# Kernel tuning notes

Hardware: AMD Instinct MI355X
Metric: run time of the kernel (lower is better)

Reference implementation:

```python
import jax, jax.numpy as jnp
import numpy as np
from jax import lax

B, FEA, C, DIM_OUT, HEADS, H, W = 4, 3, 256, 256, 8, 32, 32
EPS = 1e-5


def setup_inputs() -> dict:
    key = jax.random.key(0)
    ks = jax.random.split(key, 10)
    return {
        "x": jax.random.normal(ks[0], (B, C, H, W), jnp.float32),
        "query": jax.random.normal(ks[1], (B, FEA * H * W, C), jnp.float32),
        "conv_q_w": jax.random.normal(ks[2], (FEA, C, 1, 3, 3), jnp.float32) * 0.1,
        "bn_q_gamma": jnp.ones((FEA, C), jnp.float32),
        "bn_q_beta": jnp.zeros((FEA, C), jnp.float32),
        "bn_q_mean": jnp.zeros((FEA, C), jnp.float32),
        "bn_q_var": jnp.ones((FEA, C), jnp.float32),
        "conv_k_w": jax.random.normal(ks[3], (C, 1, 3, 3), jnp.float32) * 0.1,
        "bn_k_gamma": jnp.ones((C,), jnp.float32),
        "bn_k_beta": jnp.zeros((C,), jnp.float32),
        "bn_k_mean": jnp.zeros((C,), jnp.float32),
        "bn_k_var": jnp.ones((C,), jnp.float32),
        "conv_v_w": jax.random.normal(ks[4], (C, 1, 3, 3), jnp.float32) * 0.1,
        "bn_v_gamma": jnp.ones((C,), jnp.float32),
        "bn_v_beta": jnp.zeros((C,), jnp.float32),
        "bn_v_mean": jnp.zeros((C,), jnp.float32),
        "bn_v_var": jnp.ones((C,), jnp.float32),
        "proj_q_w": jax.random.normal(ks[5], (DIM_OUT, C), jnp.float32) * 0.02,
        "proj_k_w": jax.random.normal(ks[6], (DIM_OUT, C), jnp.float32) * 0.02,
        "proj_v_w": jax.random.normal(ks[7], (DIM_OUT, C), jnp.float32) * 0.02,
        "proj_w": jax.random.normal(ks[8], (DIM_OUT, DIM_OUT), jnp.float32) * 0.02,
        "proj_b": jnp.zeros((DIM_OUT,), jnp.float32),
        "h": H,
        "w": W,
    }


def _dw_conv_bn(x, w, gamma, beta, mean, var):
    # x: [B, C, H, W]; w: [C, 1, 3, 3] depthwise; BN in eval mode (running stats)
    y = lax.conv_general_dilated(
        x, w, window_strides=(1, 1), padding="SAME",
        feature_group_count=x.shape[1],
        dimension_numbers=("NCHW", "OIHW", "NCHW"))
    inv = gamma * lax.rsqrt(var + EPS)
    return y * inv[None, :, None, None] + (beta - mean * inv)[None, :, None, None]


def reference(x, query, conv_q_w, bn_q_gamma, bn_q_beta, bn_q_mean, bn_q_var,
              conv_k_w, bn_k_gamma, bn_k_beta, bn_k_mean, bn_k_var,
              conv_v_w, bn_v_gamma, bn_v_beta, bn_v_mean, bn_v_var,
              proj_q_w, proj_k_w, proj_v_w, proj_w, proj_b, h, w):
    b, c = x.shape[0], x.shape[1]
    res = h * w
    # split query into fea_no maps, depthwise conv + BN each, concat tokens
    q_parts = []
    for i in range(FEA):
        qi = query[:, res * i:res * (i + 1), :].reshape(b, h, w, c).transpose(0, 3, 1, 2)
        qi = _dw_conv_bn(qi, conv_q_w[i], bn_q_gamma[i], bn_q_beta[i], bn_q_mean[i], bn_q_var[i])
        q_parts.append(qi.reshape(b, c, res).transpose(0, 2, 1))  # [B, h*w, C]
    q_tok = jnp.concatenate(q_parts, axis=1)                      # [B, FEA*h*w, C]
    k_tok = _dw_conv_bn(x, conv_k_w, bn_k_gamma, bn_k_beta, bn_k_mean, bn_k_var)
    k_tok = k_tok.reshape(b, c, res).transpose(0, 2, 1)           # [B, h*w, C]
    v_tok = _dw_conv_bn(x, conv_v_w, bn_v_gamma, bn_v_beta, bn_v_mean, bn_v_var)
    v_tok = v_tok.reshape(b, c, res).transpose(0, 2, 1)
    hd = DIM_OUT // HEADS
    q = (q_tok @ proj_q_w.T).reshape(b, -1, HEADS, hd).transpose(0, 2, 1, 3)  # [B,H,L,d]
    k = (k_tok @ proj_k_w.T).reshape(b, -1, HEADS, hd).transpose(0, 2, 1, 3)  # [B,H,T,d]
    v = (v_tok @ proj_v_w.T).reshape(b, -1, HEADS, hd).transpose(0, 2, 1, 3)
    scale = DIM_OUT ** (-0.5)  # note: original scales by dim_out, not head_dim
    attn = jax.nn.softmax(jnp.einsum("bhld,bhtd->bhlt", q, k) * scale, axis=-1)
    out = jnp.einsum("bhlt,bhtd->bhld", attn, v)
    out = out.transpose(0, 2, 1, 3).reshape(b, -1, DIM_OUT)
    return out @ proj_w.T + proj_b
```

## Files before the change

### kernel.cpp

```cpp
#include <hip/hip_runtime.h>
#include <hip/hip_bf16.h>
#include <math.h>

#define B_     4
#define C_     256
#define RES_   1024
#define FEA_   3
#define LQ_    3072
#define HEADS_ 8
#define EPS_   1e-5f

typedef __bf16 bf16x8 __attribute__((ext_vector_type(8)));
typedef float  f32x16 __attribute__((ext_vector_type(16)));
typedef unsigned int uint4e __attribute__((ext_vector_type(4)));

#if __has_builtin(__builtin_amdgcn_exp2f)
#define EXP2(x) __builtin_amdgcn_exp2f(x)
#else
#define EXP2(x) exp2f(x)
#endif

__device__ __forceinline__ unsigned short bfbits(float v) {
    return __builtin_bit_cast(unsigned short, (__bf16)v);
}
__device__ __forceinline__ unsigned int pkbf(float lo, float hi2) {
    return (unsigned int)bfbits(lo) | ((unsigned int)bfbits(hi2) << 16);
}

__global__ __launch_bounds__(256) void pre_kernel(
    const float* __restrict__ query, const float* __restrict__ x,
    const float* __restrict__ wq,
    const float* __restrict__ gq, const float* __restrict__ bq,
    const float* __restrict__ mq, const float* __restrict__ vq,
    const float* __restrict__ wk, const float* __restrict__ gk, const float* __restrict__ bk,
    const float* __restrict__ mk, const float* __restrict__ vk,
    const float* __restrict__ wv, const float* __restrict__ gv, const float* __restrict__ bv,
    const float* __restrict__ mv, const float* __restrict__ vv,
    const float* __restrict__ pw0, const float* __restrict__ pw1,
    const float* __restrict__ pw2, const float* __restrict__ pw3,
    __bf16* __restrict__ q_tok, float* __restrict__ k_tok, float* __restrict__ v_tok,
    __bf16* __restrict__ Wq, __bf16* __restrict__ Wk,
    __bf16* __restrict__ Wv, __bf16* __restrict__ Wo)
{
    __shared__ float plane[RES_];
    int blk = blockIdx.x, tid = threadIdx.x;

    if (blk < 3072) {
        int b = blk / 768, rem = blk % 768;
        int part = rem >> 8, rem2 = rem & 255;
        int y = rem2 >> 3, x0 = (rem2 & 7) * 4;
        int c = tid;
        const float* wp = wq + (size_t)(part * 256 + c) * 9;
        const float* qb = query + ((size_t)b * LQ_ + (size_t)part * 1024) * 256 + c;

        float w[9];
#pragma unroll
        for (int i = 0; i < 9; ++i) w[i] = wp[i];

        float v[3][6];
#pragma unroll
        for (int ky = 0; ky < 3; ++ky) {
            int yy = y + ky - 1;
#pragma unroll
            for (int kx = 0; kx < 6; ++kx) {
                int xx = x0 - 1 + kx;
                bool ok = ((unsigned)yy < 32u) && ((unsigned)xx < 32u);
                v[ky][kx] = ok ? qb[(size_t)(yy * 32 + xx) * 256] : 0.f;
            }
        }
        int gi = part * 256 + c;
        float inv = gq[gi] * rsqrtf(vq[gi] + EPS_);
        float sh  = bq[gi] - mq[gi] * inv;
#pragma unroll
        for (int xi = 0; xi < 4; ++xi) {
            float acc = 0.f;
#pragma unroll
            for (int ky = 0; ky < 3; ++ky)
#pragma unroll
                for (int kj = 0; kj < 3; ++kj)
                    acc = fmaf(w[ky * 3 + kj], v[ky][xi + kj], acc);
            int l = part * 1024 + y * 32 + x0 + xi;
            q_tok[((size_t)b * LQ_ + l) * 256 + c] = (__bf16)fmaf(acc, inv, sh);
        }
    } else if (blk < 5120) {
        int idx = blk - 3072;
        int c = idx & 255, b = (idx >> 8) & 3, which = idx >> 10;
        const float* xp = x + ((size_t)b * 256 + c) * RES_;
#pragma unroll
        for (int i = 0; i < 4; ++i) plane[tid + i * 256] = xp[tid + i * 256];
        __syncthreads();

        const float* wp = (which ? wv : wk) + (size_t)c * 9;
        float w[9];
#pragma unroll
        for (int i = 0; i < 9; ++i) w[i] = wp[i];
        float inv = (which ? gv : gk)[c] * rsqrtf((which ? vv : vk)[c] + EPS_);
        float sh  = (which ? bv : bk)[c] - (which ? mv : mk)[c] * inv;
        float* out = (which ? v_tok : k_tok) + ((size_t)b * 256 + c) * RES_;
#pragma unroll
        for (int i0 = 0; i0 < 4; ++i0) {
            int p = tid + i0 * 256;
            int y = p >> 5, xx = p & 31;
            float acc = 0.f;
#pragma unroll
            for (int ky = 0; ky < 3; ++ky) {
                int yy = y + ky - 1;
                if ((unsigned)yy >= 32u) continue;
#pragma unroll
                for (int kx = 0; kx < 3; ++kx) {
                    int x2 = xx + kx - 1;
                    if ((unsigned)x2 >= 32u) continue;
                    acc = fmaf(w[ky * 3 + kx], plane[yy * 32 + x2], acc);
                }
            }
            out[p] = fmaf(acc, inv, sh);
        }
    } else {
        int idx = blk - 5120;
        int m = idx >> 6;
        const float* s = m == 0 ? pw0 : m == 1 ? pw1 : m == 2 ? pw2 : pw3;
        __bf16*      d = m == 0 ? Wq  : m == 1 ? Wk  : m == 2 ? Wv  : Wo;
        int i = ((idx & 63) * 256 + tid) * 4;
        float4 v = *(const float4*)(s + i);
        ushort4 u;
        u.x = bfbits(v.x); u.y = bfbits(v.y); u.z = bfbits(v.z); u.w = bfbits(v.w);
        *(ushort4*)(d + i) = u;
    }
}

__global__ __launch_bounds__(256) void gemm_qkv_kernel(
    const __bf16* __restrict__ qt, const float* __restrict__ kt, const float* __restrict__ vt,
    const __bf16* __restrict__ Wq, const __bf16* __restrict__ Wk, const __bf16* __restrict__ Wv,
    __bf16* __restrict__ Qb, __bf16* __restrict__ Kb, __bf16* __restrict__ VT)
{
    int tid = threadIdx.x, lane = tid & 63, l31 = lane & 31, hi = lane >> 5;
    int gid = blockIdx.x * 4 + (tid >> 6);

    f32x16 acc;
#pragma unroll
    for (int r = 0; r < 16; ++r) acc[r] = 0.f;

    if (gid < 3072) {
        int b = gid / 768, rem = gid % 768;
        int j0 = (rem >> 3) * 32, i0 = (rem & 7) * 32;
        const __bf16* Bp = qt + ((size_t)b * LQ_ + j0 + l31) * 256 + 8 * hi;
        const __bf16* Ap = Wq + (size_t)(i0 + l31) * 256 + 8 * hi;
#pragma unroll
        for (int k0 = 0; k0 < 256; k0 += 16) {
            acc = __builtin_amdgcn_mfma_f32_32x32x16_bf16(
                *(const bf16x8*)(Ap + k0), *(const bf16x8*)(Bp + k0), acc, 0, 0, 0);
        }
        const float scale = 0.0625f * 1.44269504f;
        int head = i0 >> 5;
        __bf16* op = Qb + ((size_t)(b * HEADS_ + head) * LQ_ + j0 + l31) * 32 + 4 * hi;
#pragma unroll
        for (int rr = 0; rr < 4; ++rr) {
            ushort4 u;
            u.x = bfbits(acc[4 * rr + 0] * scale); u.y = bfbits(acc[4 * rr + 1] * scale);
            u.z = bfbits(acc[4 * rr + 2] * scale); u.w = bfbits(acc[4 * rr + 3] * scale);
            *(ushort4*)(op + 8 * rr) = u;
        }
    } else if (gid < 4096) {
        int g = gid - 3072;
        int b = g >> 8, rem = g & 255;
        int j0 = (rem >> 3) * 32, i0 = (rem & 7) * 32;
        const float* Bbase = kt + (size_t)b * 256 * RES_ + j0 + l31;
        const __bf16* Ap = Wk + (size_t)(i0 + l31) * 256 + 8 * hi;
#pragma unroll
        for (int k0 = 0; k0 < 256; k0 += 16) {
            bf16x8 bfr;
#pragma unroll
            for (int jj = 0; jj < 8; ++jj)
                bfr[jj] = (__bf16)Bbase[(size_t)(k0 + 8 * hi + jj) * RES_];
            acc = __builtin_amdgcn_mfma_f32_32x32x16_bf16(
                *(const bf16x8*)(Ap + k0), bfr, acc, 0, 0, 0);
        }
        int head = i0 >> 5;
        __bf16* op = Kb + ((size_t)(b * HEADS_ + head) * RES_ + j0 + l31) * 32 + 4 * hi;
#pragma unroll
        for (int rr = 0; rr < 4; ++rr) {
            ushort4 u;
            u.x = bfbits(acc[4 * rr + 0]); u.y = bfbits(acc[4 * rr + 1]);
            u.z = bfbits(acc[4 * rr + 2]); u.w = bfbits(acc[4 * rr + 3]);
            *(ushort4*)(op + 8 * rr) = u;
        }
    } else {
        int g = gid - 4096;
        int b = g >> 8, rem = g & 255;
        int i0t = (rem >> 3) * 32, j0 = (rem & 7) * 32;
        const float* Abase = vt + (size_t)b * 256 * RES_ + i0t + l31;
        const __bf16* Bp = Wv + (size_t)(j0 + l31) * 256 + 8 * hi;
#pragma unroll
        for (int k0 = 0; k0 < 256; k0 += 16) {
            bf16x8 afr;
#pragma unroll
            for (int jj = 0; jj < 8; ++jj)
                afr[jj] = (__bf16)Abase[(size_t)(k0 + 8 * hi + jj) * RES_];
            acc = __builtin_amdgcn_mfma_f32_32x32x16_bf16(
                afr, *(const bf16x8*)(Bp + k0), acc, 0, 0, 0);
        }
        int head = j0 >> 5;
        __bf16* op = VT + ((size_t)(b * HEADS_ + head) * 32 + l31) * RES_ + i0t + 4 * hi;
#pragma unroll
        for (int rr = 0; rr < 4; ++rr) {
            ushort4 u;
            u.x = bfbits(acc[4 * rr + 0]); u.y = bfbits(acc[4 * rr + 1]);
            u.z = bfbits(acc[4 * rr + 2]); u.w = bfbits(acc[4 * rr + 3]);
            *(ushort4*)(op + 8 * rr) = u;
        }
    }
}

__global__ __launch_bounds__(256) void gemm_out_kernel(
    const __bf16* __restrict__ Oc, const __bf16* __restrict__ Wo,
    const float* __restrict__ bias, float* __restrict__ out)
{
    int tid = threadIdx.x, lane = tid & 63, l31 = lane & 31, hi = lane >> 5;
    int gid = blockIdx.x * 4 + (tid >> 6);
    int b = gid / 768, rem = gid % 768;
    int j0 = (rem >> 3) * 32, i0 = (rem & 7) * 32;
    const __bf16* Bp = Oc + ((size_t)b * LQ_ + j0 + l31) * 256 + 8 * hi;
    const __bf16* Ap = Wo + (size_t)(i0 + l31) * 256 + 8 * hi;

    f32x16 acc;
#pragma unroll
    for (int r = 0; r < 16; ++r) acc[r] = 0.f;
#pragma unroll
    for (int k0 = 0; k0 < 256; k0 += 16) {
        acc = __builtin_amdgcn_mfma_f32_32x32x16_bf16(
            *(const bf16x8*)(Ap + k0), *(const bf16x8*)(Bp + k0), acc, 0, 0, 0);
    }
    float* op = out + ((size_t)b * LQ_ + j0 + l31) * 256 + i0 + 4 * hi;
#pragma unroll
    for (int rr = 0; rr < 4; ++rr) {
        float4 bv = *(const float4*)(bias + i0 + 4 * hi + 8 * rr);
        float4 r4;
        r4.x = acc[4 * rr + 0] + bv.x; r4.y = acc[4 * rr + 1] + bv.y;
        r4.z = acc[4 * rr + 2] + bv.z; r4.w = acc[4 * rr + 3] + bv.w;
        *(float4*)(op + 8 * rr) = r4;
    }
}

__global__ __launch_bounds__(256) void attn_mfma_kernel(
    const __bf16* __restrict__ Qb, const __bf16* __restrict__ Kb,
    const __bf16* __restrict__ VT, __bf16* __restrict__ Oc)
{
    __shared__ float Os[3][64][35];
    int tid  = threadIdx.x;
    int lane = tid & 63, l31 = lane & 31, hi = lane >> 5;
    int th   = tid >> 6;

    int i    = blockIdx.x;
    int xcd  = i & 7, slot = i >> 3;
    int bh   = xcd * 4 + slot / 48;
    int q0   = (slot % 48) * 64;

    const __bf16* qpA = Qb + ((size_t)bh * LQ_ + q0 + l31) * 32 + 8 * hi;
    bf16x8 qA0 = *(const bf16x8*)qpA;
    bf16x8 qA1 = *(const bf16x8*)(qpA + 16);
    bf16x8 qB0 = *(const bf16x8*)(qpA + 1024);
    bf16x8 qB1 = *(const bf16x8*)(qpA + 1040);

    const __bf16* kp = Kb + ((size_t)bh * RES_ + th * 256 + l31) * 32 + 8 * hi;
    const __bf16* vp = VT + ((size_t)bh * 32 + l31) * RES_ + th * 256 + 8 * hi;

    f32x16 oA, oB;
#pragma unroll
    for (int r = 0; r < 16; ++r) { oA[r] = 0.f; oB[r] = 0.f; }
    float lsA = 0.f, lsB = 0.f;

    auto smpack = [&](const f32x16& s, float& ls, bf16x8& pb1, bf16x8& pb2) {
        float p[16];
#pragma unroll
        for (int r = 0; r < 16; ++r) p[r] = EXP2(s[r]);
#pragma unroll
        for (int r = 0; r < 16; ++r) ls += p[r];

        unsigned int w0 = pkbf(p[0],  p[1]),  w1 = pkbf(p[2],  p[3]);
        unsigned int w2 = pkbf(p[4],  p[5]),  w3 = pkbf(p[6],  p[7]);
        unsigned int w4 = pkbf(p[8],  p[9]),  w5 = pkbf(p[10], p[11]);
        unsigned int w6 = pkbf(p[12], p[13]), w7 = pkbf(p[14], p[15]);

        asm("v_permlane32_swap_b32 %0, %1" : "+v"(w0), "+v"(w2));
        asm("v_permlane32_swap_b32 %0, %1" : "+v"(w1), "+v"(w3));
        asm("v_permlane32_swap_b32 %0, %1" : "+v"(w4), "+v"(w6));
        asm("v_permlane32_swap_b32 %0, %1" : "+v"(w5), "+v"(w7));

        uint4e b1 = { w0, w1, w2, w3 };
        uint4e b2 = { w4, w5, w6, w7 };
        pb1 = __builtin_bit_cast(bf16x8, b1);
        pb2 = __builtin_bit_cast(bf16x8, b2);
    };

#pragma unroll
    for (int st = 0; st < 8; ++st) {
        const __bf16* kc = kp + (size_t)st * 1024;
        const __bf16* vc = vp + (size_t)st * 32;
        bf16x8 K0 = *(const bf16x8*)kc;
        bf16x8 K1 = *(const bf16x8*)(kc + 16);
        bf16x8 V0 = *(const bf16x8*)vc;
        bf16x8 V1 = *(const bf16x8*)(vc + 16);

        f32x16 sA, sB;
#pragma unroll
        for (int r = 0; r < 16; ++r) { sA[r] = 0.f; sB[r] = 0.f; }
        sA = __builtin_amdgcn_mfma_f32_32x32x16_bf16(K0, qA0, sA, 0, 0, 0);
        sB = __builtin_amdgcn_mfma_f32_32x32x16_bf16(K0, qB0, sB, 0, 0, 0);
        sA = __builtin_amdgcn_mfma_f32_32x32x16_bf16(K1, qA1, sA, 0, 0, 0);
        sB = __builtin_amdgcn_mfma_f32_32x32x16_bf16(K1, qB1, sB, 0, 0, 0);

        bf16x8 pA1, pA2, pB1, pB2;
        smpack(sA, lsA, pA1, pA2);
        smpack(sB, lsB, pB1, pB2);

        oA = __builtin_amdgcn_mfma_f32_32x32x16_bf16(V0, pA1, oA, 0, 0, 0);
        oB = __builtin_amdgcn_mfma_f32_32x32x16_bf16(V0, pB1, oB, 0, 0, 0);
        oA = __builtin_amdgcn_mfma_f32_32x32x16_bf16(V1, pA2, oA, 0, 0, 0);
        oB = __builtin_amdgcn_mfma_f32_32x32x16_bf16(V1, pB2, oB, 0, 0, 0);
    }

    lsA += __shfl_xor(lsA, 32, 64);
    lsB += __shfl_xor(lsB, 32, 64);

    if (th) {
#pragma unroll
        for (int r = 0; r < 16; ++r) {
            Os[th - 1][lane][r]      = oA[r];
            Os[th - 1][lane][17 + r] = oB[r];
        }
        Os[th - 1][lane][16] = lsA;
        Os[th - 1][lane][33] = lsB;
    }
    __syncthreads();
    if (!th) {
        int b = bh >> 3, h = bh & 7;
        float lA = lsA + Os[0][lane][16] + Os[1][lane][16] + Os[2][lane][16];
        float lB = lsB + Os[0][lane][33] + Os[1][lane][33] + Os[2][lane][33];
        float invA = 1.0f / lA, invB = 1.0f / lB;
        __bf16* opA = Oc + ((size_t)b * LQ_ + q0 + l31) * 256 + h * 32 + 4 * hi;
        __bf16* opB = opA + (size_t)32 * 256;
#pragma unroll
        for (int rr = 0; rr < 4; ++rr) {
            ushort4 ua, ub;
            ua.x = bfbits((oA[4*rr+0] + Os[0][lane][4*rr+0] + Os[1][lane][4*rr+0] + Os[2][lane][4*rr+0]) * invA);
            ua.y = bfbits((oA[4*rr+1] + Os[0][lane][4*rr+1] + Os[1][lane][4*rr+1] + Os[2][lane][4*rr+1]) * invA);
            ua.z = bfbits((oA[4*rr+2] + Os[0][lane][4*rr+2] + Os[1][lane][4*rr+2] + Os[2][lane][4*rr+2]) * invA);
            ua.w = bfbits((oA[4*rr+3] + Os[0][lane][4*rr+3] + Os[1][lane][4*rr+3] + Os[2][lane][4*rr+3]) * invA);
            ub.x = bfbits((oB[4*rr+0] + Os[0][lane][17+4*rr+0] + Os[1][lane][17+4*rr+0] + Os[2][lane][17+4*rr+0]) * invB);
            ub.y = bfbits((oB[4*rr+1] + Os[0][lane][17+4*rr+1] + Os[1][lane][17+4*rr+1] + Os[2][lane][17+4*rr+1]) * invB);
            ub.z = bfbits((oB[4*rr+2] + Os[0][lane][17+4*rr+2] + Os[1][lane][17+4*rr+2] + Os[2][lane][17+4*rr+2]) * invB);
            ub.w = bfbits((oB[4*rr+3] + Os[0][lane][17+4*rr+3] + Os[1][lane][17+4*rr+3] + Os[2][lane][17+4*rr+3]) * invB);
            *(ushort4*)(opA + 8 * rr) = ua;
            *(ushort4*)(opB + 8 * rr) = ub;
        }
    }
}

extern "C" void kernel_launch(void* const* d_in, const int* in_sizes, int n_in,
                              void* d_out, int out_size, void* d_ws, size_t ws_size,
                              hipStream_t stream) {
    const float* x        = (const float*)d_in[0];
    const float* query    = (const float*)d_in[1];
    const float* conv_q_w = (const float*)d_in[2];
    const float* bn_q_g   = (const float*)d_in[3];
    const float* bn_q_b   = (const float*)d_in[4];
    const float* bn_q_m   = (const float*)d_in[5];
    const float* bn_q_v   = (const float*)d_in[6];
    const float* conv_k_w = (const float*)d_in[7];
    const float* bn_k_g   = (const float*)d_in[8];
    const float* bn_k_b   = (const float*)d_in[9];
    const float* bn_k_m   = (const float*)d_in[10];
    const float* bn_k_v   = (const float*)d_in[11];
    const float* conv_v_w = (const float*)d_in[12];
    const float* bn_v_g   = (const float*)d_in[13];
    const float* bn_v_b   = (const float*)d_in[14];
    const float* bn_v_m   = (const float*)d_in[15];
    const float* bn_v_v   = (const float*)d_in[16];
    const float* proj_q_w = (const float*)d_in[17];
    const float* proj_k_w = (const float*)d_in[18];
    const float* proj_v_w = (const float*)d_in[19];
    const float* proj_w   = (const float*)d_in[20];
    const float* proj_b   = (const float*)d_in[21];

    char* ws = (char*)d_ws;
    __bf16* q_tok = (__bf16*)(ws + 0);
    float*  k_tok = (float*) (ws + 6291456);
    float*  v_tok = (float*) (ws + 10485760);
    __bf16* Qb    = (__bf16*)(ws + 14680064);
    __bf16* Kb    = (__bf16*)(ws + 20971520);
    __bf16* VT    = (__bf16*)(ws + 23068672);
    __bf16* Wq    = (__bf16*)(ws + 25165824);
    __bf16* Wk    = (__bf16*)(ws + 25296896);
    __bf16* Wv    = (__bf16*)(ws + 25427968);
    __bf16* Wo    = (__bf16*)(ws + 25559040);
    __bf16* Oc    = q_tok;
    float*  out   = (float*)d_out;

    pre_kernel<<<dim3(5376), 256, 0, stream>>>(
        query, x, conv_q_w, bn_q_g, bn_q_b, bn_q_m, bn_q_v,
        conv_k_w, bn_k_g, bn_k_b, bn_k_m, bn_k_v,
        conv_v_w, bn_v_g, bn_v_b, bn_v_m, bn_v_v,
        proj_q_w, proj_k_w, proj_v_w, proj_w,
        q_tok, k_tok, v_tok, Wq, Wk, Wv, Wo);

    gemm_qkv_kernel<<<dim3(1280), 256, 0, stream>>>(
        q_tok, k_tok, v_tok, Wq, Wk, Wv, Qb, Kb, VT);

    attn_mfma_kernel<<<dim3(1536), 256, 0, stream>>>(Qb, Kb, VT, Oc);

    gemm_out_kernel<<<dim3(768), 256, 0, stream>>>(Oc, Wo, proj_b, out);
}
```

Measured before the change: 79.96 us.

## Tile query depthwise conv 4x4 per thread and prefetch K in attention loop

```diff
diff --git a/kernel.cpp b/kernel.cpp
--- a/kernel.cpp
+++ b/kernel.cpp
@@ -45,10 +45,10 @@
     __shared__ float plane[RES_];
     int blk = blockIdx.x, tid = threadIdx.x;
 
-    if (blk < 3072) {
-        int b = blk / 768, rem = blk % 768;
-        int part = rem >> 8, rem2 = rem & 255;
-        int y = rem2 >> 3, x0 = (rem2 & 7) * 4;
+    if (blk < 768) {
+        int b = blk / 192, rem = blk % 192;
+        int part = rem >> 6, t = rem & 63;
+        int y0 = (t >> 3) * 4, x0 = (t & 7) * 4;
         int c = tid;
         const float* wp = wq + (size_t)(part * 256 + c) * 9;
         const float* qb = query + ((size_t)b * LQ_ + (size_t)part * 1024) * 256 + c;
@@ -57,33 +57,36 @@
 #pragma unroll
         for (int i = 0; i < 9; ++i) w[i] = wp[i];
 
-        float v[3][6];
-#pragma unroll
-        for (int ky = 0; ky < 3; ++ky) {
-            int yy = y + ky - 1;
-#pragma unroll
-            for (int kx = 0; kx < 6; ++kx) {
-                int xx = x0 - 1 + kx;
+        float v[6][6];
+#pragma unroll
+        for (int iy = 0; iy < 6; ++iy) {
+            int yy = y0 - 1 + iy;
+#pragma unroll
+            for (int ix = 0; ix < 6; ++ix) {
+                int xx = x0 - 1 + ix;
                 bool ok = ((unsigned)yy < 32u) && ((unsigned)xx < 32u);
-                v[ky][kx] = ok ? qb[(size_t)(yy * 32 + xx) * 256] : 0.f;
+                v[iy][ix] = ok ? qb[(size_t)(yy * 32 + xx) * 256] : 0.f;
             }
         }
         int gi = part * 256 + c;
         float inv = gq[gi] * rsqrtf(vq[gi] + EPS_);
         float sh  = bq[gi] - mq[gi] * inv;
 #pragma unroll
-        for (int xi = 0; xi < 4; ++xi) {
-            float acc = 0.f;
-#pragma unroll
-            for (int ky = 0; ky < 3; ++ky)
-#pragma unroll
-                for (int kj = 0; kj < 3; ++kj)
-                    acc = fmaf(w[ky * 3 + kj], v[ky][xi + kj], acc);
-            int l = part * 1024 + y * 32 + x0 + xi;
-            q_tok[((size_t)b * LQ_ + l) * 256 + c] = (__bf16)fmaf(acc, inv, sh);
-        }
-    } else if (blk < 5120) {
-        int idx = blk - 3072;
+        for (int yi = 0; yi < 4; ++yi) {
+#pragma unroll
+            for (int xi = 0; xi < 4; ++xi) {
+                float acc = 0.f;
+#pragma unroll
+                for (int ky = 0; ky < 3; ++ky)
+#pragma unroll
+                    for (int kj = 0; kj < 3; ++kj)
+                        acc = fmaf(w[ky * 3 + kj], v[yi + ky][xi + kj], acc);
+                int l = part * 1024 + (y0 + yi) * 32 + x0 + xi;
+                q_tok[((size_t)b * LQ_ + l) * 256 + c] = (__bf16)fmaf(acc, inv, sh);
+            }
+        }
+    } else if (blk < 2816) {
+        int idx = blk - 768;
         int c = idx & 255, b = (idx >> 8) & 3, which = idx >> 10;
         const float* xp = x + ((size_t)b * 256 + c) * RES_;
 #pragma unroll
@@ -116,7 +119,7 @@
             out[p] = fmaf(acc, inv, sh);
         }
     } else {
-        int idx = blk - 5120;
+        int idx = blk - 2816;
         int m = idx >> 6;
         const float* s = m == 0 ? pw0 : m == 1 ? pw1 : m == 2 ? pw2 : pw3;
         __bf16*      d = m == 0 ? Wq  : m == 1 ? Wk  : m == 2 ? Wv  : Wo;
@@ -292,31 +295,44 @@
         pb2 = __builtin_bit_cast(bf16x8, b2);
     };
 
+    bf16x8 kc0 = *(const bf16x8*)kp;
+    bf16x8 kc1 = *(const bf16x8*)(kp + 16);
+
 #pragma unroll
     for (int st = 0; st < 8; ++st) {
-        const __bf16* kc = kp + (size_t)st * 1024;
         const __bf16* vc = vp + (size_t)st * 32;
-        bf16x8 K0 = *(const bf16x8*)kc;
-        bf16x8 K1 = *(const bf16x8*)(kc + 16);
         bf16x8 V0 = *(const bf16x8*)vc;
         bf16x8 V1 = *(const bf16x8*)(vc + 16);
 
+        bf16x8 kn0, kn1;
+        if (st < 7) {
+            const __bf16* kn = kp + (size_t)(st + 1) * 1024;
+            kn0 = *(const bf16x8*)kn;
+            kn1 = *(const bf16x8*)(kn + 16);
+        }
+
         f32x16 sA, sB;
 #pragma unroll
         for (int r = 0; r < 16; ++r) { sA[r] = 0.f; sB[r] = 0.f; }
-        sA = __builtin_amdgcn_mfma_f32_32x32x16_bf16(K0, qA0, sA, 0, 0, 0);
-        sB = __builtin_amdgcn_mfma_f32_32x32x16_bf16(K0, qB0, sB, 0, 0, 0);
-        sA = __builtin_amdgcn_mfma_f32_32x32x16_bf16(K1, qA1, sA, 0, 0, 0);
-        sB = __builtin_amdgcn_mfma_f32_32x32x16_bf16(K1, qB1, sB, 0, 0, 0);
+        __builtin_amdgcn_s_setprio(1);
+        sA = __builtin_amdgcn_mfma_f32_32x32x16_bf16(kc0, qA0, sA, 0, 0, 0);
+        sB = __builtin_amdgcn_mfma_f32_32x32x16_bf16(kc0, qB0, sB, 0, 0, 0);
+        sA = __builtin_amdgcn_mfma_f32_32x32x16_bf16(kc1, qA1, sA, 0, 0, 0);
+        sB = __builtin_amdgcn_mfma_f32_32x32x16_bf16(kc1, qB1, sB, 0, 0, 0);
+        __builtin_amdgcn_s_setprio(0);
 
         bf16x8 pA1, pA2, pB1, pB2;
         smpack(sA, lsA, pA1, pA2);
         smpack(sB, lsB, pB1, pB2);
 
+        __builtin_amdgcn_s_setprio(1);
         oA = __builtin_amdgcn_mfma_f32_32x32x16_bf16(V0, pA1, oA, 0, 0, 0);
         oB = __builtin_amdgcn_mfma_f32_32x32x16_bf16(V0, pB1, oB, 0, 0, 0);
         oA = __builtin_amdgcn_mfma_f32_32x32x16_bf16(V1, pA2, oA, 0, 0, 0);
         oB = __builtin_amdgcn_mfma_f32_32x32x16_bf16(V1, pB2, oB, 0, 0, 0);
+        __builtin_amdgcn_s_setprio(0);
+
+        if (st < 7) { kc0 = kn0; kc1 = kn1; }
     }
 
     lsA += __shfl_xor(lsA, 32, 64);
@@ -396,7 +412,7 @@
     __bf16* Oc    = q_tok;
     float*  out   = (float*)d_out;
 
-    pre_kernel<<<dim3(5376), 256, 0, stream>>>(
+    pre_kernel<<<dim3(3072), 256, 0, stream>>>(
         query, x, conv_q_w, bn_q_g, bn_q_b, bn_q_m, bn_q_v,
         conv_k_w, bn_k_g, bn_k_b, bn_k_m, bn_k_v,
         conv_v_w, bn_v_g, bn_v_b, bn_v_m, bn_v_v,
```

New measurement: 79.34 us. About the same (-0.8%).
